# Optimization experiments

Hardware: AMD Instinct MI355X
Metric: run time of the kernel (lower is better)

## Reference

```python
import jax, jax.numpy as jnp
import numpy as np

B, MAXF, NFEAT, FT_OUT = 16384, 32, 768, 1024

def setup_inputs() -> dict:
    key = jax.random.key(0)
    k1, k2, k3, k4, k5, k6 = jax.random.split(key, 6)
    values = jnp.ones((B, MAXF), dtype=jnp.float32)
    stm_indices = jax.random.randint(k1, (B, MAXF), 0, NFEAT, dtype=jnp.int32)
    nstm_indices = jax.random.randint(k2, (B, MAXF), 0, NFEAT, dtype=jnp.int32)
    ft_w = jax.random.normal(k3, (NFEAT, FT_OUT), dtype=jnp.float32) * 0.02
    ft_b = jax.random.normal(k4, (FT_OUT,), dtype=jnp.float32) * 0.02
    out_w = jax.random.normal(k5, (2 * FT_OUT, 1), dtype=jnp.float32) * 0.02
    out_b = jax.random.normal(k6, (1,), dtype=jnp.float32) * 0.02
    return {"values": values, "stm_indices": stm_indices, "nstm_indices": nstm_indices,
            "ft_w": ft_w, "ft_b": ft_b, "out_w": out_w, "out_b": out_b}

def _ft_slice(indices, values, ft_w, ft_b):
    # sparse gather-accumulate: [B, MAXF] indices into [NFEAT, FT_OUT] table
    gathered = jnp.take(ft_w, indices, axis=0)          # [B, MAXF, FT_OUT]
    return jnp.einsum('bf,bfd->bd', values, gathered) + ft_b  # [B, FT_OUT]

def reference(values, stm_indices, nstm_indices, ft_w, ft_b, out_w, out_b):
    stm_ft = _ft_slice(stm_indices, values, ft_w, ft_b)
    nstm_ft = _ft_slice(nstm_indices, values, ft_w, ft_b)
    hidden = jnp.clip(jnp.concatenate([stm_ft, nstm_ft], axis=1), 0.0, 1.0)
    return jax.nn.sigmoid(hidden @ out_w + out_b)  # [B, 1]
```

## Files before the change

kernel.cpp:

```cpp
#include <hip/hip_runtime.h>
#include <hip/hip_fp16.h>
#include <math.h>

#define BATCH 16384
#define MAXF 32
#define NFEAT 768
#define FT_OUT 1024
#define CHUNK 32
#define NCHUNK (FT_OUT / CHUNK)
#define GROUPS 24
#define CH_HALVES (NFEAT * CHUNK)

#define GET4(a, f) (((f) & 3) == 0 ? (a)[(f) >> 2].x : \
                    ((f) & 3) == 1 ? (a)[(f) >> 2].y : \
                    ((f) & 3) == 2 ? (a)[(f) >> 2].z : (a)[(f) >> 2].w)

typedef unsigned int uint_t;

__global__ __launch_bounds__(256, 3) void nnboard_main(
    const float* __restrict__ values,
    const int*   __restrict__ stm_idx,
    const int*   __restrict__ nstm_idx,
    const float* __restrict__ ft_w,
    const float* __restrict__ ft_b,
    const float* __restrict__ out_w,
    float*       __restrict__ partials)
{
    __shared__ __half s_tab[CH_HALVES];

    const int tid = threadIdx.x;
    const int c = blockIdx.x % NCHUNK;
    const int g = blockIdx.x / NCHUNK;
    const __half2 zero2 = __float2half2_rn(0.f);

    {
        const int lane8 = tid & 7;
        const int rbase = tid >> 3;
        #pragma unroll
        for (int k = 0; k < NFEAT / 32; ++k) {
            const int r = k * 32 + rbase;
            const float4 f = *(const float4*)(ft_w + (size_t)r * FT_OUT + c * CHUNK + lane8 * 4);
            __half2 h0 = __floats2half2_rn(f.x, f.y);
            __half2 h1 = __floats2half2_rn(f.z, f.w);
            uint2 u;
            u.x = *reinterpret_cast<uint_t*>(&h0);
            u.y = *reinterpret_cast<uint_t*>(&h1);
            *(uint2*)(s_tab + r * CHUNK + lane8 * 4) = u;
        }
    }
    __syncthreads();

    const int grp = tid >> 2;
    const int j   = tid & 3;
    const int col0 = c * CHUNK + j * 8;
    const __half* my_tab = s_tab + j * 8;

    const float4 bia0 = *(const float4*)(ft_b + col0);
    const float4 bia1 = *(const float4*)(ft_b + col0 + 4);
    const float4 ws0  = *(const float4*)(out_w + col0);
    const float4 ws1  = *(const float4*)(out_w + col0 + 4);
    const float4 wn0  = *(const float4*)(out_w + FT_OUT + col0);
    const float4 wn1  = *(const float4*)(out_w + FT_OUT + col0 + 4);

    for (int it = g; it < BATCH / 64; it += GROUPS) {
        const int b = it * 64 + grp;

        const int4*   sp = (const int4*)(stm_idx + b * MAXF);
        const int4*   np = (const int4*)(nstm_idx + b * MAXF);
        const float4* vp = (const float4*)(values + b * MAXF);
        int4 si[8], ni[8];
        float4 vv[8];
        #pragma unroll
        for (int k = 0; k < 8; ++k) { si[k] = sp[k]; ni[k] = np[k]; vv[k] = vp[k]; }

        __half2 accs[4] = {zero2, zero2, zero2, zero2};
        __half2 accn[4] = {zero2, zero2, zero2, zero2};

        #pragma unroll
        for (int f = 0; f < MAXF; ++f) {
            const int is = GET4(si, f);
            const int in = GET4(ni, f);
            const __half2 v2 = __float2half2_rn(GET4(vv, f));
            const uint4 qs = *(const uint4*)(my_tab + is * CHUNK);
            const uint4 qn = *(const uint4*)(my_tab + in * CHUNK);
            accs[0] = __hfma2(*(const __half2*)&qs.x, v2, accs[0]);
            accs[1] = __hfma2(*(const __half2*)&qs.y, v2, accs[1]);
            accs[2] = __hfma2(*(const __half2*)&qs.z, v2, accs[2]);
            accs[3] = __hfma2(*(const __half2*)&qs.w, v2, accs[3]);
            accn[0] = __hfma2(*(const __half2*)&qn.x, v2, accn[0]);
            accn[1] = __hfma2(*(const __half2*)&qn.y, v2, accn[1]);
            accn[2] = __hfma2(*(const __half2*)&qn.z, v2, accn[2]);
            accn[3] = __hfma2(*(const __half2*)&qn.w, v2, accn[3]);
        }

        float p = 0.f;
        {
            const float2 f0 = __half22float2(accs[0]);
            const float2 f1 = __half22float2(accs[1]);
            const float2 f2 = __half22float2(accs[2]);
            const float2 f3 = __half22float2(accs[3]);
            const float2 g0 = __half22float2(accn[0]);
            const float2 g1 = __half22float2(accn[1]);
            const float2 g2 = __half22float2(accn[2]);
            const float2 g3 = __half22float2(accn[3]);
            auto clip = [](float x) { return fminf(fmaxf(x, 0.f), 1.f); };
            p = fmaf(clip(f0.x + bia0.x), ws0.x, p);
            p = fmaf(clip(f0.y + bia0.y), ws0.y, p);
            p = fmaf(clip(f1.x + bia0.z), ws0.z, p);
            p = fmaf(clip(f1.y + bia0.w), ws0.w, p);
            p = fmaf(clip(f2.x + bia1.x), ws1.x, p);
            p = fmaf(clip(f2.y + bia1.y), ws1.y, p);
            p = fmaf(clip(f3.x + bia1.z), ws1.z, p);
            p = fmaf(clip(f3.y + bia1.w), ws1.w, p);
            p = fmaf(clip(g0.x + bia0.x), wn0.x, p);
            p = fmaf(clip(g0.y + bia0.y), wn0.y, p);
            p = fmaf(clip(g1.x + bia0.z), wn0.z, p);
            p = fmaf(clip(g1.y + bia0.w), wn0.w, p);
            p = fmaf(clip(g2.x + bia1.x), wn1.x, p);
            p = fmaf(clip(g2.y + bia1.y), wn1.y, p);
            p = fmaf(clip(g3.x + bia1.z), wn1.z, p);
            p = fmaf(clip(g3.y + bia1.w), wn1.w, p);
        }

        p += __shfl_down(p, 1, 64);
        p += __shfl_down(p, 2, 64);
        if (j == 0) partials[c * BATCH + b] = p;
    }
}

__global__ __launch_bounds__(256) void reduce_sigmoid_kernel(
    const float* __restrict__ partials,
    const float* __restrict__ out_b,
    float* __restrict__ out)
{
    const int i = blockIdx.x * 256 + threadIdx.x;
    float s = out_b[0];
    #pragma unroll
    for (int k = 0; k < NCHUNK; ++k)
        s += partials[k * BATCH + i];
    out[i] = 1.f / (1.f + expf(-s));
}

extern "C" void kernel_launch(void* const* d_in, const int* in_sizes, int n_in,
                              void* d_out, int out_size, void* d_ws, size_t ws_size,
                              hipStream_t stream) {
    const float* values   = (const float*)d_in[0];
    const int*   stm_idx  = (const int*)d_in[1];
    const int*   nstm_idx = (const int*)d_in[2];
    const float* ft_w     = (const float*)d_in[3];
    const float* ft_b     = (const float*)d_in[4];
    const float* out_w    = (const float*)d_in[5];
    const float* out_b    = (const float*)d_in[6];
    float*       out      = (float*)d_out;

    float* partials = (float*)d_ws;

    nnboard_main<<<NCHUNK * GROUPS, 256, 0, stream>>>(
        values, stm_idx, nstm_idx, ft_w, ft_b, out_w, partials);
    reduce_sigmoid_kernel<<<BATCH / 256, 256, 0, stream>>>(partials, out_b, out);
}
```

Before: 110.4 us.

## Store feature table in LDS as e5m2 bytes and widen per-thread columns

The per-chunk feature-transformer table is converted to 8-bit e5m2 instead of fp16 and expanded to half2 with byte permutes before each hfma2. Each thread now covers 16 columns, so a row is handled by two threads instead of four, and occupancy and group count are raised. This halves LDS footprint and the number of LDS bytes read per gathered row, and it amortizes index loads over more columns. The trade-off is extra permute instructions and much coarser weight precision, which may exceed accuracy tolerance.

```diff
diff --git a/kernel.cpp b/kernel.cpp
--- a/kernel.cpp
+++ b/kernel.cpp
@@ -8,8 +8,8 @@
 #define FT_OUT 1024
 #define CHUNK 32
 #define NCHUNK (FT_OUT / CHUNK)
-#define GROUPS 24
-#define CH_HALVES (NFEAT * CHUNK)
+#define GROUPS 32
+#define CH_BYTES (NFEAT * CHUNK)
 
 #define GET4(a, f) (((f) & 3) == 0 ? (a)[(f) >> 2].x : \
                     ((f) & 3) == 1 ? (a)[(f) >> 2].y : \
@@ -17,7 +17,24 @@
 
 typedef unsigned int uint_t;
 
-__global__ __launch_bounds__(256, 3) void nnboard_main(
+__device__ __forceinline__ uint_t rne_e5m2(float w) {
+    unsigned short h = __half_as_ushort(__float2half(w));
+    unsigned short t = (unsigned short)(h + 0x7F + ((h >> 8) & 1));
+    return (uint_t)(t >> 8) & 0xFFu;
+}
+__device__ __forceinline__ uint_t pack4_e5m2(float4 f) {
+    return rne_e5m2(f.x) | (rne_e5m2(f.y) << 8) |
+           (rne_e5m2(f.z) << 16) | (rne_e5m2(f.w) << 24);
+}
+__device__ __forceinline__ void fma4_bf8(uint_t q, __half2 v2,
+                                         __half2& a0, __half2& a1) {
+    uint_t lo = __builtin_amdgcn_perm(q, q, 0x010C000Cu);
+    uint_t hi = __builtin_amdgcn_perm(q, q, 0x030C020Cu);
+    a0 = __hfma2(*reinterpret_cast<__half2*>(&lo), v2, a0);
+    a1 = __hfma2(*reinterpret_cast<__half2*>(&hi), v2, a1);
+}
+
+__global__ __launch_bounds__(256, 4) void nnboard_main(
     const float* __restrict__ values,
     const int*   __restrict__ stm_idx,
     const int*   __restrict__ nstm_idx,
@@ -26,7 +43,7 @@
     const float* __restrict__ out_w,
     float*       __restrict__ partials)
 {
-    __shared__ __half s_tab[CH_HALVES];
+    __shared__ __align__(16) unsigned char s_tab[CH_BYTES];
 
     const int tid = threadIdx.x;
     const int c = blockIdx.x % NCHUNK;
@@ -40,30 +57,26 @@
         for (int k = 0; k < NFEAT / 32; ++k) {
             const int r = k * 32 + rbase;
             const float4 f = *(const float4*)(ft_w + (size_t)r * FT_OUT + c * CHUNK + lane8 * 4);
-            __half2 h0 = __floats2half2_rn(f.x, f.y);
-            __half2 h1 = __floats2half2_rn(f.z, f.w);
-            uint2 u;
-            u.x = *reinterpret_cast<uint_t*>(&h0);
-            u.y = *reinterpret_cast<uint_t*>(&h1);
-            *(uint2*)(s_tab + r * CHUNK + lane8 * 4) = u;
+            *(uint_t*)(s_tab + r * CHUNK + lane8 * 4) = pack4_e5m2(f);
         }
     }
     __syncthreads();
 
-    const int grp = tid >> 2;
-    const int j   = tid & 3;
-    const int col0 = c * CHUNK + j * 8;
-    const __half* my_tab = s_tab + j * 8;
+    const int grp = tid >> 1;
+    const int j   = tid & 1;
+    const int col0 = c * CHUNK + j * 16;
+    const unsigned char* my_tab = s_tab + j * 16;
 
-    const float4 bia0 = *(const float4*)(ft_b + col0);
-    const float4 bia1 = *(const float4*)(ft_b + col0 + 4);
-    const float4 ws0  = *(const float4*)(out_w + col0);
-    const float4 ws1  = *(const float4*)(out_w + col0 + 4);
-    const float4 wn0  = *(const float4*)(out_w + FT_OUT + col0);
-    const float4 wn1  = *(const float4*)(out_w + FT_OUT + col0 + 4);
+    float4 bia[4], ws[4], wn[4];
+    #pragma unroll
+    for (int k = 0; k < 4; ++k) {
+        bia[k] = *(const float4*)(ft_b + col0 + 4 * k);
+        ws[k]  = *(const float4*)(out_w + col0 + 4 * k);
+        wn[k]  = *(const float4*)(out_w + FT_OUT + col0 + 4 * k);
+    }
 
-    for (int it = g; it < BATCH / 64; it += GROUPS) {
-        const int b = it * 64 + grp;
+    for (int it = g; it < BATCH / 128; it += GROUPS) {
+        const int b = it * 128 + grp;
 
         const int4*   sp = (const int4*)(stm_idx + b * MAXF);
         const int4*   np = (const int4*)(nstm_idx + b * MAXF);
@@ -73,8 +86,8 @@
         #pragma unroll
         for (int k = 0; k < 8; ++k) { si[k] = sp[k]; ni[k] = np[k]; vv[k] = vp[k]; }
 
-        __half2 accs[4] = {zero2, zero2, zero2, zero2};
-        __half2 accn[4] = {zero2, zero2, zero2, zero2};
+        __half2 accs[8] = {zero2, zero2, zero2, zero2, zero2, zero2, zero2, zero2};
+        __half2 accn[8] = {zero2, zero2, zero2, zero2, zero2, zero2, zero2, zero2};
 
         #pragma unroll
         for (int f = 0; f < MAXF; ++f) {
@@ -83,47 +96,37 @@
             const __half2 v2 = __float2half2_rn(GET4(vv, f));
             const uint4 qs = *(const uint4*)(my_tab + is * CHUNK);
             const uint4 qn = *(const uint4*)(my_tab + in * CHUNK);
-            accs[0] = __hfma2(*(const __half2*)&qs.x, v2, accs[0]);
-            accs[1] = __hfma2(*(const __half2*)&qs.y, v2, accs[1]);
-            accs[2] = __hfma2(*(const __half2*)&qs.z, v2, accs[2]);
-            accs[3] = __hfma2(*(const __half2*)&qs.w, v2, accs[3]);
-            accn[0] = __hfma2(*(const __half2*)&qn.x, v2, accn[0]);
-            accn[1] = __hfma2(*(const __half2*)&qn.y, v2, accn[1]);
-            accn[2] = __hfma2(*(const __half2*)&qn.z, v2, accn[2]);
-            accn[3] = __hfma2(*(const __half2*)&qn.w, v2, accn[3]);
+            fma4_bf8(qs.x, v2, accs[0], accs[1]);
+            fma4_bf8(qs.y, v2, accs[2], accs[3]);
+            fma4_bf8(qs.z, v2, accs[4], accs[5]);
+            fma4_bf8(qs.w, v2, accs[6], accs[7]);
+            fma4_bf8(qn.x, v2, accn[0], accn[1]);
+            fma4_bf8(qn.y, v2, accn[2], accn[3]);
+            fma4_bf8(qn.z, v2, accn[4], accn[5]);
+            fma4_bf8(qn.w, v2, accn[6], accn[7]);
         }
 
         float p = 0.f;
         {
-            const float2 f0 = __half22float2(accs[0]);
-            const float2 f1 = __half22float2(accs[1]);
-            const float2 f2 = __half22float2(accs[2]);
-            const float2 f3 = __half22float2(accs[3]);
-            const float2 g0 = __half22float2(accn[0]);
-            const float2 g1 = __half22float2(accn[1]);
-            const float2 g2 = __half22float2(accn[2]);
-            const float2 g3 = __half22float2(accn[3]);
             auto clip = [](float x) { return fminf(fmaxf(x, 0.f), 1.f); };
-            p = fmaf(clip(f0.x + bia0.x), ws0.x, p);
-            p = fmaf(clip(f0.y + bia0.y), ws0.y, p);
-            p = fmaf(clip(f1.x + bia0.z), ws0.z, p);
-            p = fmaf(clip(f1.y + bia0.w), ws0.w, p);
-            p = fmaf(clip(f2.x + bia1.x), ws1.x, p);
-            p = fmaf(clip(f2.y + bia1.y), ws1.y, p);
-            p = fmaf(clip(f3.x + bia1.z), ws1.z, p);
-            p = fmaf(clip(f3.y + bia1.w), ws1.w, p);
-            p = fmaf(clip(g0.x + bia0.x), wn0.x, p);
-            p = fmaf(clip(g0.y + bia0.y), wn0.y, p);
-            p = fmaf(clip(g1.x + bia0.z), wn0.z, p);
-            p = fmaf(clip(g1.y + bia0.w), wn0.w, p);
-            p = fmaf(clip(g2.x + bia1.x), wn1.x, p);
-            p = fmaf(clip(g2.y + bia1.y), wn1.y, p);
-            p = fmaf(clip(g3.x + bia1.z), wn1.z, p);
-            p = fmaf(clip(g3.y + bia1.w), wn1.w, p);
+            #pragma unroll
+            for (int k = 0; k < 4; ++k) {
+                const float2 s0 = __half22float2(accs[2 * k]);
+                const float2 s1 = __half22float2(accs[2 * k + 1]);
+                const float2 n0 = __half22float2(accn[2 * k]);
+                const float2 n1 = __half22float2(accn[2 * k + 1]);
+                p = fmaf(clip(s0.x + bia[k].x), ws[k].x, p);
+                p = fmaf(clip(s0.y + bia[k].y), ws[k].y, p);
+                p = fmaf(clip(s1.x + bia[k].z), ws[k].z, p);
+                p = fmaf(clip(s1.y + bia[k].w), ws[k].w, p);
+                p = fmaf(clip(n0.x + bia[k].x), wn[k].x, p);
+                p = fmaf(clip(n0.y + bia[k].y), wn[k].y, p);
+                p = fmaf(clip(n1.x + bia[k].z), wn[k].z, p);
+                p = fmaf(clip(n1.y + bia[k].w), wn[k].w, p);
+            }
         }
 
         p += __shfl_down(p, 1, 64);
-        p += __shfl_down(p, 2, 64);
         if (j == 0) partials[c * BATCH + b] = p;
     }
 }
```

After: 116.8 us. 1.06x slower.

## Store feature-transform table slice in LDS as e5m2 bytes instead of fp16

Applied to the files above, without the earlier changes.

Quantizes each block's weight slice to 8-bit e5m2 when staging into shared memory, then expands to fp16 with byte permutes before packed half FMAs. This halves LDS footprint and gather bandwidth, so occupancy is raised to four blocks per CU and the group count increases. The cost is much coarser weight precision (two mantissa bits) and extra permute instructions per gathered row.

```diff
diff --git a/kernel.cpp b/kernel.cpp
--- a/kernel.cpp
+++ b/kernel.cpp
@@ -8,8 +8,8 @@
 #define FT_OUT 1024
 #define CHUNK 32
 #define NCHUNK (FT_OUT / CHUNK)
-#define GROUPS 24
-#define CH_HALVES (NFEAT * CHUNK)
+#define GROUPS 32
+#define CH_BYTES (NFEAT * CHUNK)
 
 #define GET4(a, f) (((f) & 3) == 0 ? (a)[(f) >> 2].x : \
                     ((f) & 3) == 1 ? (a)[(f) >> 2].y : \
@@ -17,7 +17,24 @@
 
 typedef unsigned int uint_t;
 
-__global__ __launch_bounds__(256, 3) void nnboard_main(
+__device__ __forceinline__ uint_t rne_e5m2(float w) {
+    unsigned short h = __half_as_ushort(__float2half(w));
+    unsigned short t = (unsigned short)(h + 0x7F + ((h >> 8) & 1));
+    return (uint_t)(t >> 8) & 0xFFu;
+}
+__device__ __forceinline__ uint_t pack4_e5m2(float4 f) {
+    return rne_e5m2(f.x) | (rne_e5m2(f.y) << 8) |
+           (rne_e5m2(f.z) << 16) | (rne_e5m2(f.w) << 24);
+}
+__device__ __forceinline__ void fma4_bf8(uint_t q, __half2 v2,
+                                         __half2& a0, __half2& a1) {
+    uint_t lo = __builtin_amdgcn_perm(q, q, 0x010C000Cu);
+    uint_t hi = __builtin_amdgcn_perm(q, q, 0x030C020Cu);
+    a0 = __hfma2(*reinterpret_cast<__half2*>(&lo), v2, a0);
+    a1 = __hfma2(*reinterpret_cast<__half2*>(&hi), v2, a1);
+}
+
+__global__ __launch_bounds__(256, 4) void nnboard_main(
     const float* __restrict__ values,
     const int*   __restrict__ stm_idx,
     const int*   __restrict__ nstm_idx,
@@ -26,7 +43,7 @@
     const float* __restrict__ out_w,
     float*       __restrict__ partials)
 {
-    __shared__ __half s_tab[CH_HALVES];
+    __shared__ __align__(16) unsigned char s_tab[CH_BYTES];
 
     const int tid = threadIdx.x;
     const int c = blockIdx.x % NCHUNK;
@@ -40,12 +57,7 @@
         for (int k = 0; k < NFEAT / 32; ++k) {
             const int r = k * 32 + rbase;
             const float4 f = *(const float4*)(ft_w + (size_t)r * FT_OUT + c * CHUNK + lane8 * 4);
-            __half2 h0 = __floats2half2_rn(f.x, f.y);
-            __half2 h1 = __floats2half2_rn(f.z, f.w);
-            uint2 u;
-            u.x = *reinterpret_cast<uint_t*>(&h0);
-            u.y = *reinterpret_cast<uint_t*>(&h1);
-            *(uint2*)(s_tab + r * CHUNK + lane8 * 4) = u;
+            *(uint_t*)(s_tab + r * CHUNK + lane8 * 4) = pack4_e5m2(f);
         }
     }
     __syncthreads();
@@ -53,7 +65,7 @@
     const int grp = tid >> 2;
     const int j   = tid & 3;
     const int col0 = c * CHUNK + j * 8;
-    const __half* my_tab = s_tab + j * 8;
+    const unsigned char* my_tab = s_tab + j * 8;
 
     const float4 bia0 = *(const float4*)(ft_b + col0);
     const float4 bia1 = *(const float4*)(ft_b + col0 + 4);
@@ -81,16 +93,12 @@
             const int is = GET4(si, f);
             const int in = GET4(ni, f);
             const __half2 v2 = __float2half2_rn(GET4(vv, f));
-            const uint4 qs = *(const uint4*)(my_tab + is * CHUNK);
-            const uint4 qn = *(const uint4*)(my_tab + in * CHUNK);
-            accs[0] = __hfma2(*(const __half2*)&qs.x, v2, accs[0]);
-            accs[1] = __hfma2(*(const __half2*)&qs.y, v2, accs[1]);
-            accs[2] = __hfma2(*(const __half2*)&qs.z, v2, accs[2]);
-            accs[3] = __hfma2(*(const __half2*)&qs.w, v2, accs[3]);
-            accn[0] = __hfma2(*(const __half2*)&qn.x, v2, accn[0]);
-            accn[1] = __hfma2(*(const __half2*)&qn.y, v2, accn[1]);
-            accn[2] = __hfma2(*(const __half2*)&qn.z, v2, accn[2]);
-            accn[3] = __hfma2(*(const __half2*)&qn.w, v2, accn[3]);
+            const uint2 qs = *(const uint2*)(my_tab + is * CHUNK);
+            const uint2 qn = *(const uint2*)(my_tab + in * CHUNK);
+            fma4_bf8(qs.x, v2, accs[0], accs[1]);
+            fma4_bf8(qs.y, v2, accs[2], accs[3]);
+            fma4_bf8(qn.x, v2, accn[0], accn[1]);
+            fma4_bf8(qn.y, v2, accn[2], accn[3]);
         }
 
         float p = 0.f;
```

After: 123.2 us. +11.6%, slower.

## Duplicate LDS table with parity-based copy selection to cut bank conflicts

Applied to the files above, without the earlier changes.

Stores two copies of the half-precision weight chunk in shared memory, offset by one row. Each lane picks a copy from the parity of its row index and its batch-row parity. The goal is to spread random-gather LDS reads over more banks and reduce conflicts. Blocks grow to 512 threads with one block per CU and 16 stripes, so the grid shrinks from 768 to 512 blocks. The shared footprint doubles to about 96KB, which limits occupancy to one block and adds extra shared stores during the table fill.

```diff
diff --git a/kernel.cpp b/kernel.cpp
--- a/kernel.cpp
+++ b/kernel.cpp
@@ -8,8 +8,10 @@
 #define FT_OUT 1024
 #define CHUNK 32
 #define NCHUNK (FT_OUT / CHUNK)
-#define GROUPS 24
+#define STRIPES 16
+#define THREADS 512
 #define CH_HALVES (NFEAT * CHUNK)
+#define DUPOFF (CH_HALVES + CHUNK)
 
 #define GET4(a, f) (((f) & 3) == 0 ? (a)[(f) >> 2].x : \
                     ((f) & 3) == 1 ? (a)[(f) >> 2].y : \
@@ -17,7 +19,7 @@
 
 typedef unsigned int uint_t;
 
-__global__ __launch_bounds__(256, 3) void nnboard_main(
+__global__ __launch_bounds__(THREADS, 1) void nnboard_main(
     const float* __restrict__ values,
     const int*   __restrict__ stm_idx,
     const int*   __restrict__ nstm_idx,
@@ -26,7 +28,7 @@
     const float* __restrict__ out_w,
     float*       __restrict__ partials)
 {
-    __shared__ __half s_tab[CH_HALVES];
+    __shared__ __half s_tab[DUPOFF + CH_HALVES];
 
     const int tid = threadIdx.x;
     const int c = blockIdx.x % NCHUNK;
@@ -37,8 +39,8 @@
         const int lane8 = tid & 7;
         const int rbase = tid >> 3;
         #pragma unroll
-        for (int k = 0; k < NFEAT / 32; ++k) {
-            const int r = k * 32 + rbase;
+        for (int k = 0; k < NFEAT / 64; ++k) {
+            const int r = k * 64 + rbase;
             const float4 f = *(const float4*)(ft_w + (size_t)r * FT_OUT + c * CHUNK + lane8 * 4);
             __half2 h0 = __floats2half2_rn(f.x, f.y);
             __half2 h1 = __floats2half2_rn(f.z, f.w);
@@ -46,14 +48,15 @@
             u.x = *reinterpret_cast<uint_t*>(&h0);
             u.y = *reinterpret_cast<uint_t*>(&h1);
             *(uint2*)(s_tab + r * CHUNK + lane8 * 4) = u;
+            *(uint2*)(s_tab + DUPOFF + r * CHUNK + lane8 * 4) = u;
         }
     }
     __syncthreads();
 
     const int grp = tid >> 2;
     const int j   = tid & 3;
+    const int p   = grp & 1;
     const int col0 = c * CHUNK + j * 8;
-    const __half* my_tab = s_tab + j * 8;
 
     const float4 bia0 = *(const float4*)(ft_b + col0);
     const float4 bia1 = *(const float4*)(ft_b + col0 + 4);
@@ -62,8 +65,8 @@
     const float4 wn0  = *(const float4*)(out_w + FT_OUT + col0);
     const float4 wn1  = *(const float4*)(out_w + FT_OUT + col0 + 4);
 
-    for (int it = g; it < BATCH / 64; it += GROUPS) {
-        const int b = it * 64 + grp;
+    for (int it = g; it < BATCH / 128; it += STRIPES) {
+        const int b = it * 128 + grp;
 
         const int4*   sp = (const int4*)(stm_idx + b * MAXF);
         const int4*   np = (const int4*)(nstm_idx + b * MAXF);
@@ -81,8 +84,10 @@
             const int is = GET4(si, f);
             const int in = GET4(ni, f);
             const __half2 v2 = __float2half2_rn(GET4(vv, f));
-            const uint4 qs = *(const uint4*)(my_tab + is * CHUNK);
-            const uint4 qn = *(const uint4*)(my_tab + in * CHUNK);
+            const int os = is * CHUNK + ((is ^ p) & 1) * DUPOFF + j * 8;
+            const int on = in * CHUNK + ((in ^ p) & 1) * DUPOFF + j * 8;
+            const uint4 qs = *(const uint4*)(s_tab + os);
+            const uint4 qn = *(const uint4*)(s_tab + on);
             accs[0] = __hfma2(*(const __half2*)&qs.x, v2, accs[0]);
             accs[1] = __hfma2(*(const __half2*)&qs.y, v2, accs[1]);
             accs[2] = __hfma2(*(const __half2*)&qs.z, v2, accs[2]);
@@ -93,7 +98,7 @@
             accn[3] = __hfma2(*(const __half2*)&qn.w, v2, accn[3]);
         }
 
-        float p = 0.f;
+        float p_out = 0.f;
         {
             const float2 f0 = __half22float2(accs[0]);
             const float2 f1 = __half22float2(accs[1]);
@@ -104,27 +109,27 @@
             const float2 g2 = __half22float2(accn[2]);
             const float2 g3 = __half22float2(accn[3]);
             auto clip = [](float x) { return fminf(fmaxf(x, 0.f), 1.f); };
-            p = fmaf(clip(f0.x + bia0.x), ws0.x, p);
-            p = fmaf(clip(f0.y + bia0.y), ws0.y, p);
-            p = fmaf(clip(f1.x + bia0.z), ws0.z, p);
-            p = fmaf(clip(f1.y + bia0.w), ws0.w, p);
-            p = fmaf(clip(f2.x + bia1.x), ws1.x, p);
-            p = fmaf(clip(f2.y + bia1.y), ws1.y, p);
-            p = fmaf(clip(f3.x + bia1.z), ws1.z, p);
-            p = fmaf(clip(f3.y + bia1.w), ws1.w, p);
-            p = fmaf(clip(g0.x + bia0.x), wn0.x, p);
-            p = fmaf(clip(g0.y + bia0.y), wn0.y, p);
-            p = fmaf(clip(g1.x + bia0.z), wn0.z, p);
-            p = fmaf(clip(g1.y + bia0.w), wn0.w, p);
-            p = fmaf(clip(g2.x + bia1.x), wn1.x, p);
-            p = fmaf(clip(g2.y + bia1.y), wn1.y, p);
-            p = fmaf(clip(g3.x + bia1.z), wn1.z, p);
-            p = fmaf(clip(g3.y + bia1.w), wn1.w, p);
+            p_out = fmaf(clip(f0.x + bia0.x), ws0.x, p_out);
+            p_out = fmaf(clip(f0.y + bia0.y), ws0.y, p_out);
+            p_out = fmaf(clip(f1.x + bia0.z), ws0.z, p_out);
+            p_out = fmaf(clip(f1.y + bia0.w), ws0.w, p_out);
+            p_out = fmaf(clip(f2.x + bia1.x), ws1.x, p_out);
+            p_out = fmaf(clip(f2.y + bia1.y), ws1.y, p_out);
+            p_out = fmaf(clip(f3.x + bia1.z), ws1.z, p_out);
+            p_out = fmaf(clip(f3.y + bia1.w), ws1.w, p_out);
+            p_out = fmaf(clip(g0.x + bia0.x), wn0.x, p_out);
+            p_out = fmaf(clip(g0.y + bia0.y), wn0.y, p_out);
+            p_out = fmaf(clip(g1.x + bia0.z), wn0.z, p_out);
+            p_out = fmaf(clip(g1.y + bia0.w), wn0.w, p_out);
+            p_out = fmaf(clip(g2.x + bia1.x), wn1.x, p_out);
+            p_out = fmaf(clip(g2.y + bia1.y), wn1.y, p_out);
+            p_out = fmaf(clip(g3.x + bia1.z), wn1.z, p_out);
+            p_out = fmaf(clip(g3.y + bia1.w), wn1.w, p_out);
         }
 
-        p += __shfl_down(p, 1, 64);
-        p += __shfl_down(p, 2, 64);
-        if (j == 0) partials[c * BATCH + b] = p;
+        p_out += __shfl_down(p_out, 1, 64);
+        p_out += __shfl_down(p_out, 2, 64);
+        if (j == 0) partials[c * BATCH + b] = p_out;
     }
 }
 
@@ -155,7 +160,7 @@
 
     float* partials = (float*)d_ws;
 
-    nnboard_main<<<NCHUNK * GROUPS, 256, 0, stream>>>(
+    nnboard_main<<<NCHUNK * STRIPES, THREADS, 0, stream>>>(
         values, stm_idx, nstm_idx, ft_w, ft_b, out_w, partials);
     reduce_sigmoid_kernel<<<BATCH / 256, 256, 0, stream>>>(partials, out_b, out);
 }
```

After: 131.1 us. +18.8%, slower.
